# Kernel optimization log

Hardware: AMD Instinct MI355X
Metric: run time of the kernel (lower is better)

The kernel has to match this reference:

```python
import jax, jax.numpy as jnp
import numpy as np

Lx, Ly = 10, 10          # PEPS lattice (contract split at Lx//2 as in source)
PHYS, D, CHI = 2, 4, 4   # physical dim, bond dim, boundary max_bond (chi = D)


def setup_inputs() -> dict:
    key = jax.random.key(0)
    k1, k2 = jax.random.split(key)
    # scale so each site tensor has Frobenius norm ~1.5 (keeps the contraction
    # value inside float32 range; quimb handles this via equalize_norms=1.0)
    scale = 1.5 / np.sqrt(PHYS * D ** 4)
    peps = jax.random.normal(k1, (Lx, Ly, PHYS, D, D, D, D), dtype=jnp.float32) * scale
    x = jax.random.randint(k2, (Lx * Ly,), 0, PHYS, dtype=jnp.int32)
    return {"peps": peps, "x": x}


def _site(peps, x, i, j):
    # isel: select physical index; realize open boundary by slicing edge bonds to 1
    T = jnp.take(peps[i, j], x[i * Ly + j], axis=0)  # [Du, Dr, Dd, Dl]
    if i == Lx - 1:
        T = T[:1]
    if j == Ly - 1:
        T = T[:, :1]
    if i == 0:
        T = T[:, :, :1]
    if j == 0:
        T = T[:, :, :, :1]
    return T


def _compress(mps, chi):
    """Canonical MPS compression to bond dim chi (cutoff=0, canonize=True).
    Each tensor has legs (l, r, p) where p is the dangling (up/down) leg.
    Returns compressed MPS with tensor norms stripped into a log accumulator
    (equalize_norms=1.0 semantics; reabsorbed at the end)."""
    mps = list(mps)
    n = len(mps)
    # left-to-right QR canonization
    for j in range(n - 1):
        l, r, u = mps[j].shape
        M = mps[j].transpose(0, 2, 1).reshape(l * u, r)
        Q, R = jnp.linalg.qr(M)
        k = Q.shape[1]
        mps[j] = Q.reshape(l, u, k).transpose(0, 2, 1)
        mps[j + 1] = jnp.einsum('kr,rsu->ksu', R, mps[j + 1])
    # right-to-left truncating SVD sweep
    for j in range(n - 1, 0, -1):
        l, r, u = mps[j].shape
        M = mps[j].reshape(l, r * u)
        U, S, Vh = jnp.linalg.svd(M, full_matrices=False)
        k = min(chi, S.shape[0])
        mps[j] = Vh[:k].reshape(k, r, u)
        mps[j - 1] = jnp.einsum('lmu,mk->lku', mps[j - 1], U[:, :k] * S[:k])
    # equalize norms: strip per-tensor norms into an exponent
    logZ = jnp.zeros((), mps[0].dtype)
    for j in range(n):
        nrm = jnp.linalg.norm(mps[j])
        safe = jnp.where(nrm > 0, nrm, 1.0)
        mps[j] = mps[j] / safe
        logZ = logZ + jnp.log(safe)
    return mps, logZ


def _amp(peps, x):
    logZ = jnp.zeros((), peps.dtype)
    # bottom boundary MPS from row 0: site [U,R,d=1,L] -> (l, r, u)
    bot = [_site(peps, x, 0, j)[:, :, 0].transpose(2, 1, 0) for j in range(Ly)]
    for i in range(1, Lx // 2):  # contract_boundary_from_xmin_, xrange [0, Lx//2-1]
        row = []
        for j in range(Ly):
            T = _site(peps, x, i, j)      # [U, R, d, L]
            B = bot[j]                    # [l, r, u]
            C = jnp.einsum('lru,URuL->lLrRU', B, T)
            row.append(C.reshape(B.shape[0] * T.shape[3],
                                 B.shape[1] * T.shape[1], T.shape[0]))
        bot, lz = _compress(row, CHI)
        logZ = logZ + lz
    # top boundary MPS from row Lx-1: site [U=1,R,D,L] -> (l, r, d)
    top = [_site(peps, x, Lx - 1, j)[0].transpose(2, 0, 1) for j in range(Ly)]
    for i in range(Lx - 2, Lx // 2 - 1, -1):  # contract_boundary_from_xmax_
        row = []
        for j in range(Ly):
            T = _site(peps, x, i, j)      # [U, R, D, L]
            A = top[j]                    # [l, r, d]
            C = jnp.einsum('lrd,dRDL->lLrRD', A, T)
            row.append(C.reshape(A.shape[0] * T.shape[3],
                                 A.shape[1] * T.shape[1], T.shape[2]))
        top, lz = _compress(row, CHI)
        logZ = logZ + lz
    # zip the two boundary MPS across the central cut
    v = jnp.ones((1, 1), peps.dtype)
    for j in range(Ly):
        v = jnp.einsum('ab,apu,bqu->pq', v, bot[j], top[j])
    return v[0, 0] * jnp.exp(logZ)


def reference(peps, x):
    return _amp(peps, x)
```

## Files before the change

### kernel.cpp

```cpp
#include <hip/hip_runtime.h>
#include <math.h>


#define NS 10

__device__ __forceinline__ double shfl_d(double x, int src) {
  union { double d; int i[2]; } u;
  u.d = x;
  u.i[0] = __shfl(u.i[0], src, 64);
  u.i[1] = __shfl(u.i[1], src, 64);
  return u.d;
}
__device__ __forceinline__ double shflx_d(double x, int m) {
  union { double d; int i[2]; } u;
  u.d = x;
  u.i[0] = __shfl_xor(u.i[0], m, 64);
  u.i[1] = __shfl_xor(u.i[1], m, 64);
  return u.d;
}
__device__ __forceinline__ double wsum64(double x) {
#pragma unroll
  for (int o = 1; o < 64; o <<= 1) x += shflx_d(x, o);
  return x;
}
#define SEL4(a, k) ((k) == 1 ? (a)[1] : (k) == 2 ? (a)[2] : (k) == 3 ? (a)[3] : (a)[0])

template <int NDMAX>
__device__ void jacobi_sym_x(const double* gw, double* vtw, double* ev,
                             int lane, int maxsweep) {
  const int i = lane >> 2, j4 = lane & 3;
  double g[4], v[4];
#pragma unroll
  for (int cc = 0; cc < 4; ++cc) {
    g[cc] = gw[i * 16 + j4 * 4 + cc];
    v[cc] = (i == j4 * 4 + cc) ? 1.0 : 0.0;
  }
  for (int sw = 0; sw < maxsweep; ++sw) {
    double off = 0.0, dsq = 0.0;
#pragma unroll
    for (int cc = 0; cc < 4; ++cc) {
      double gv = g[cc];
      if (j4 * 4 + cc == i) dsq += gv * gv; else off += gv * gv;
    }
    off = wsum64(off); dsq = wsum64(dsq);
    if (off <= dsq * 1e-22) break;
#pragma unroll
    for (int d = 1; d <= NDMAX; ++d) {
      const int hb = d >= 8 ? 3 : d >= 4 ? 2 : d >= 2 ? 1 : 0;
      double dsel = SEL4(g, i & 3);
      double psel = SEL4(g, (i & 3) ^ (d & 3));
      double t1 = shfl_d(dsel, (i << 2) + (i >> 2));
      double t3 = shfl_d(psel, (i << 2) + ((i ^ d) >> 2));
      double t2 = shfl_d(dsel, ((i ^ d) << 2) + ((i ^ d) >> 2));
      bool iq = ((i >> hb) & 1) != 0;
      double th = iq ? (t1 - t2) : (t2 - t1);
      double ph = 2.0 * t3;
      double den = fabs(th) + sqrt(th * th + ph * ph);
      double t = (den > 0.0) ? copysign(1.0, th) * ph / den : 0.0;
      double cr = rsqrt(1.0 + t * t);
      double sr = t * cr;
      double oc[4], os[4], oth[4];
#pragma unroll
      for (int cc = 0; cc < 4; ++cc) {
        int col = (j4 << 2) + cc;
        int asrc = (col << 2) + (col >> 2);
        oc[cc] = shfl_d(cr, asrc);
        os[cc] = shfl_d(sr, asrc);
        oth[cc] = (d >> 2) ? shflx_d(g[cc ^ (d & 3)], d >> 2)
                           : g[cc ^ (d & 3)];
      }
#pragma unroll
      for (int cc = 0; cc < 4; ++cc) {
        int col = (j4 << 2) + cc;
        double sg = ((col >> hb) & 1) ? os[cc] : -os[cc];
        g[cc] = oc[cc] * g[cc] + sg * oth[cc];
      }
      double og[4], ov[4];
#pragma unroll
      for (int cc = 0; cc < 4; ++cc) og[cc] = shflx_d(g[cc], d << 2);
#pragma unroll
      for (int cc = 0; cc < 4; ++cc) ov[cc] = shflx_d(v[cc], d << 2);
      double sg2 = iq ? sr : -sr;
#pragma unroll
      for (int cc = 0; cc < 4; ++cc) {
        g[cc] = cr * g[cc] + sg2 * og[cc];
        v[cc] = cr * v[cc] + sg2 * ov[cc];
      }
    }
  }
#pragma unroll
  for (int cc = 0; cc < 4; ++cc) vtw[i * 16 + j4 * 4 + cc] = v[cc];
  if ((i >> 2) == j4) ev[i] = SEL4(g, i & 3);
}

__global__ __launch_bounds__(128, 1)
void amp_kernel(const float* __restrict__ peps, const int* __restrict__ xs,
                float* __restrict__ out) {
  const int tid = threadIdx.x;
  const int team = tid >> 6;
  const int lane = tid & 63;

  __shared__ __align__(16) float Ash[2][NS][1024];
  __shared__ __align__(16) float Tmp[2][1024];
  __shared__ __align__(16) float Tsh[2][256];
  __shared__ double Rw[2][256];
  __shared__ double Gw[2][256];
  __shared__ double Vt[2][256];
  __shared__ double USw[2][64];
  __shared__ double evals[2][16];
  __shared__ int dL[2][NS], dR[2][NS];
  __shared__ double lz[2];
  __shared__ double vbuf[2][16];

  float (*A)[1024] = Ash[team];
  float* tmp = Tmp[team];
  float* tsh = Tsh[team];
  double* rw = Rw[team];
  double* gw = Gw[team];
  double* vt = Vt[team];
  double* usw = USw[team];
  double* ev = evals[team];
  int* dl = dL[team];
  int* dr = dR[team];

  double logZ = 0.0;

  {
    int row0 = team ? 9 : 0;
    for (int j = 0; j < NS; ++j) {
      int p = xs[row0 * 10 + j];
      const float* tp = peps + ((size_t)(row0 * 10 + j) * 2 + p) * 256;
      ((float4*)tsh)[lane] = ((const float4*)tp)[lane];
      __syncthreads();
      int lgLt = (j == 0) ? 0 : 2, lgRt = (j == 9) ? 0 : 2;
      int Lt = 1 << lgLt, Rt = 1 << lgRt;
      int n = Lt * Rt * 4;
      if (lane < n) {
        int ui = lane & 3, h = lane >> 2;
        int ri = h & (Rt - 1), li = h >> lgRt;
        float val = team ? tsh[ri * 16 + ui * 4 + li]
                         : tsh[ui * 64 + ri * 16 + li];
        A[j][lane] = val;
      }
      if (lane == 0) { dl[j] = Lt; dr[j] = Rt; }
      __syncthreads();
    }
  }

  for (int it = 0; it < 4; ++it) {
    int row = team ? (8 - it) : (1 + it);

    for (int j = 0; j < NS; ++j) {
      int p = xs[row * 10 + j];
      const float* tp = peps + ((size_t)(row * 10 + j) * 2 + p) * 256;
      ((float4*)tsh)[lane] = ((const float4*)tp)[lane];
      int l = dl[j], r = dr[j];
      int nb = l * r * 4;
      for (int o = lane; o < nb; o += 64) tmp[o] = A[j][o];
      __syncthreads();
      int lgLt = (j == 0) ? 0 : 2, lgRt = (j == 9) ? 0 : 2;
      int lp = l << lgLt, rp = r << lgRt;
      int lgrp = 31 - __clz(rp);
      int n = lp * rp * 4;
      for (int o = lane; o < n; o += 64) {
        int U = o & 3;
        int h = o >> 2;
        int ro = h & (rp - 1), lo = h >> lgrp;
        int li = lo >> lgLt, Li = lo & ((1 << lgLt) - 1);
        int ri = ro >> lgRt, Ri = ro & ((1 << lgRt) - 1);
        double acc = 0.0;
#pragma unroll
        for (int w = 0; w < 4; ++w) {
          float b = tmp[(li * r + ri) * 4 + w];
          float t3 = team ? tsh[w * 64 + Ri * 16 + U * 4 + Li]
                          : tsh[U * 64 + Ri * 16 + w * 4 + Li];
          acc += (double)b * (double)t3;
        }
        A[j][o] = (float)acc;
      }
      if (lane == 0) { dl[j] = lp; dr[j] = rp; }
      __syncthreads();
    }

    for (int j = 0; j < NS - 1; ++j) {
      int l = dl[j], r = dr[j];
      int rows = l * 4, cols = r;
      int kq = rows < cols ? rows : cols;
      for (int o = lane; o < 256; o += 64) rw[o] = 0.0;
      double m[16];
      int li = lane >> 2, ui = lane & 3;
      bool act = lane < rows;
#pragma unroll
      for (int c = 0; c < 16; ++c)
        m[c] = (act && c < cols) ? (double)A[j][(li * r + c) * 4 + ui] : 0.0;
      __syncthreads();
#pragma unroll
      for (int c = 0; c < 16; ++c) {
        if (c < kq) {
          double rawd[16];
#pragma unroll
          for (int c2 = c; c2 < 16; ++c2)
            if (c2 < cols) rawd[c2] = wsum64(m[c] * m[c2]);
          double nrm = sqrt(rawd[c]);
          double inv = (nrm > 1e-150) ? 1.0 / nrm : 0.0;
          m[c] *= inv;
          if (lane == 0) rw[c * 16 + c] = nrm;
#pragma unroll
          for (int c2 = c + 1; c2 < 16; ++c2) {
            if (c2 < cols) {
              double dt = rawd[c2] * inv;
              m[c2] -= dt * m[c];
              if (lane == 0) rw[c * 16 + c2] = dt;
            }
          }
        }
      }
      if (act) {
#pragma unroll
        for (int c = 0; c < 16; ++c)
          if (c < kq) A[j][(li * kq + c) * 4 + ui] = (float)m[c];
      }
      if (lane == 0) dr[j] = kq;
      __syncthreads();
      int r2 = dr[j + 1];
      int ne = cols * r2 * 4;
      for (int o = lane; o < ne; o += 64) tmp[o] = A[j + 1][o];
      __syncthreads();
      int lgr2 = 31 - __clz(r2);
      int nout = kq * r2 * 4;
      for (int o = lane; o < nout; o += 64) {
        int u2 = o & 3;
        int h = o >> 2;
        int s = h & (r2 - 1), ki = h >> lgr2;
        double acc = 0.0;
        for (int c = ki; c < cols; ++c)
          acc += rw[ki * 16 + c] * (double)tmp[(c * r2 + s) * 4 + u2];
        A[j + 1][o] = (float)acc;
      }
      if (lane == 0) dl[j + 1] = kq;
      __syncthreads();
    }

    for (int j = NS - 1; j >= 1; --j) {
      int l = dl[j], r = dr[j], ru = r * 4;
      int mdim = l < ru ? l : ru;
      int k = mdim < 4 ? mdim : 4;
      bool caseA = (l <= ru);
      int d = caseA ? l : ru;
      for (int o = lane; o < 256; o += 64) gw[o] = 0.0;
      __syncthreads();
      if (caseA) {
        int lgl = 31 - __clz(l);
        for (int idx = lane; idx < l * l; idx += 64) {
          int a = idx >> lgl, b = idx & (l - 1);
          double acc = 0.0;
          for (int t2 = 0; t2 < ru; ++t2)
            acc += (double)A[j][a * ru + t2] * (double)A[j][b * ru + t2];
          gw[a * 16 + b] = acc;
        }
      } else {
        int lgru = 31 - __clz(ru);
        for (int idx = lane; idx < ru * ru; idx += 64) {
          int a = idx >> lgru, b = idx & (ru - 1);
          double acc = 0.0;
          for (int t2 = 0; t2 < l; ++t2)
            acc += (double)A[j][t2 * ru + a] * (double)A[j][t2 * ru + b];
          gw[a * 16 + b] = acc;
        }
      }
      __syncthreads();
      if (d > 4) jacobi_sym_x<15>(gw, vt, ev, lane, 10);
      else       jacobi_sym_x<3>(gw, vt, ev, lane, 6);
      __syncthreads();
      int idxs[4]; double sv[4];
      idxs[0] = idxs[1] = idxs[2] = idxs[3] = 0;
      sv[0] = sv[1] = sv[2] = sv[3] = 0.0;
      unsigned msk = 0;
#pragma unroll
      for (int t2 = 0; t2 < 4; ++t2) {
        if (t2 < k) {
          double best = -1.0; int bi = 0;
          for (int a = 0; a < 16; ++a) {
            double ea = ev[a];
            bool ok = !((msk >> a) & 1) && (ea > best);
            best = ok ? ea : best;
            bi = ok ? a : bi;
          }
          msk |= (1u << bi);
          idxs[t2] = bi;
          sv[t2] = sqrt(best > 0.0 ? best : 0.0);
        }
      }
      double vh[4] = {0.0, 0.0, 0.0, 0.0};
      if (caseA) {
        if (lane < ru) {
#pragma unroll
          for (int t2 = 0; t2 < 4; ++t2) if (t2 < k) {
            double acc = 0.0;
            for (int a = 0; a < l; ++a)
              acc += vt[idxs[t2] * 16 + a] * (double)A[j][a * ru + lane];
            double invs = sv[t2] > 1e-150 ? 1.0 / sv[t2] : 0.0;
            vh[t2] = acc * invs;
          }
        }
        if (lane < l) {
#pragma unroll
          for (int t2 = 0; t2 < 4; ++t2)
            usw[lane * 4 + t2] =
                (t2 < k) ? vt[idxs[t2] * 16 + lane] * sv[t2] : 0.0;
        }
      } else {
        if (lane < ru) {
#pragma unroll
          for (int t2 = 0; t2 < 4; ++t2)
            if (t2 < k) vh[t2] = vt[idxs[t2] * 16 + lane];
        }
        if (lane < l) {
#pragma unroll
          for (int t2 = 0; t2 < 4; ++t2) {
            double acc = 0.0;
            if (t2 < k)
              for (int q2 = 0; q2 < ru; ++q2)
                acc += (double)A[j][lane * ru + q2] * vt[idxs[t2] * 16 + q2];
            usw[lane * 4 + t2] = acc;
          }
        }
      }
      __syncthreads();
      if (lane < ru) {
#pragma unroll
        for (int t2 = 0; t2 < 4; ++t2)
          if (t2 < k) A[j][t2 * ru + lane] = (float)vh[t2];
      }
      if (lane == 0) dl[j] = k;
      __syncthreads();
      int l1 = dl[j - 1], r1 = dr[j - 1];
      int ne = l1 * r1 * 4;
      for (int o = lane; o < ne; o += 64) tmp[o] = A[j - 1][o];
      __syncthreads();
      int lgk = 31 - __clz(k);
      int nout = l1 * k * 4;
      for (int o = lane; o < nout; o += 64) {
        int u2 = o & 3;
        int h = o >> 2;
        int ki = h & (k - 1), li2 = h >> lgk;
        double acc = 0.0;
        for (int m2 = 0; m2 < l; ++m2)
          acc += (double)tmp[(li2 * l + m2) * 4 + u2] * usw[m2 * 4 + ki];
        A[j - 1][o] = (float)acc;
      }
      if (lane == 0) dr[j - 1] = k;
      __syncthreads();
    }

    for (int j = 0; j < NS; ++j) {
      int nels = dl[j] * dr[j] * 4;
      double part = 0.0;
      for (int o = lane; o < nels; o += 64) {
        double x = A[j][o];
        part += x * x;
      }
      double nrm = sqrt(wsum64(part));
      double safe = nrm > 0.0 ? nrm : 1.0;
      float invs = (float)(1.0 / safe);
      for (int o = lane; o < nels; o += 64) A[j][o] *= invs;
      logZ += log(safe);
      __syncthreads();
    }
  }

  if (lane == 0) lz[team] = logZ;
  if (tid < 16) vbuf[0][tid] = (tid == 0) ? 1.0 : 0.0;
  __syncthreads();
  int cur = 0;
  for (int j = 0; j < NS; ++j) {
    if (tid < 16) {
      int adim = dL[0][j], pdim = dR[0][j];
      int pp = tid >> 2, qq = tid & 3;
      double acc = 0.0;
      if (pp < pdim && qq < pdim) {
        for (int a = 0; a < adim; ++a)
          for (int b = 0; b < adim; ++b) {
            double vab = vbuf[cur][a * 4 + b];
            double s2 = 0.0;
#pragma unroll
            for (int u = 0; u < 4; ++u)
              s2 += (double)Ash[0][j][(a * pdim + pp) * 4 + u] *
                    (double)Ash[1][j][(b * pdim + qq) * 4 + u];
            acc += vab * s2;
          }
      }
      vbuf[cur ^ 1][tid] = acc;
    }
    __syncthreads();
    cur ^= 1;
  }
  if (tid == 0) out[0] = (float)(vbuf[cur][0] * exp(lz[0] + lz[1]));
}

extern "C" void kernel_launch(void* const* d_in, const int* in_sizes, int n_in,
                              void* d_out, int out_size, void* d_ws, size_t ws_size,
                              hipStream_t stream) {
  const float* peps = (const float*)d_in[0];
  const int* xs = (const int*)d_in[1];
  float* out = (float*)d_out;
  (void)in_sizes; (void)n_in; (void)out_size; (void)d_ws; (void)ws_size;
  amp_kernel<<<dim3(1), dim3(128), 0, stream>>>(peps, xs, out);
}
```

Baseline: 3.559 ms.

## Vectorize LDS accesses, split accumulators, cut Jacobi sweeps and convergence reductions

Several micro-optimizations go into the boundary-contraction kernel. Shared-memory copies and row contractions now use float4 loads, dot-product loops use four independent accumulators to shorten dependency chains, and the redundant zeroing of rw is dropped. The Jacobi eigen-solver computes its threshold once, needs only one wave reduction per sweep, and runs fewer maximum sweeps. Eigenvalues are cached in registers for top-k selection. Fewer sweeps and the looser convergence test may reduce accuracy of the truncated SVD.

```diff
diff --git a/kernel.cpp b/kernel.cpp
--- a/kernel.cpp
+++ b/kernel.cpp
@@ -35,6 +35,7 @@
     g[cc] = gw[i * 16 + j4 * 4 + cc];
     v[cc] = (i == j4 * 4 + cc) ? 1.0 : 0.0;
   }
+  double thr = 0.0;
   for (int sw = 0; sw < maxsweep; ++sw) {
     double off = 0.0, dsq = 0.0;
 #pragma unroll
@@ -42,8 +43,11 @@
       double gv = g[cc];
       if (j4 * 4 + cc == i) dsq += gv * gv; else off += gv * gv;
     }
-    off = wsum64(off); dsq = wsum64(dsq);
-    if (off <= dsq * 1e-22) break;
+    if (sw == 0) {
+      thr = wsum64(off + dsq) * 1e-16;
+    } else {
+      if (wsum64(off) <= thr) break;
+    }
 #pragma unroll
     for (int d = 1; d <= NDMAX; ++d) {
       const int hb = d >= 8 ? 3 : d >= 4 ? 2 : d >= 2 ? 1 : 0;
@@ -155,8 +159,9 @@
       const float* tp = peps + ((size_t)(row * 10 + j) * 2 + p) * 256;
       ((float4*)tsh)[lane] = ((const float4*)tp)[lane];
       int l = dl[j], r = dr[j];
-      int nb = l * r * 4;
-      for (int o = lane; o < nb; o += 64) tmp[o] = A[j][o];
+      int nb4 = (l * r * 4) >> 2;
+      for (int o = lane; o < nb4; o += 64)
+        ((float4*)tmp)[o] = ((const float4*)A[j])[o];
       __syncthreads();
       int lgLt = (j == 0) ? 0 : 2, lgRt = (j == 9) ? 0 : 2;
       int lp = l << lgLt, rp = r << lgRt;
@@ -168,13 +173,16 @@
         int ro = h & (rp - 1), lo = h >> lgrp;
         int li = lo >> lgLt, Li = lo & ((1 << lgLt) - 1);
         int ri = ro >> lgRt, Ri = ro & ((1 << lgRt) - 1);
-        double acc = 0.0;
-#pragma unroll
-        for (int w = 0; w < 4; ++w) {
-          float b = tmp[(li * r + ri) * 4 + w];
-          float t3 = team ? tsh[w * 64 + Ri * 16 + U * 4 + Li]
-                          : tsh[U * 64 + Ri * 16 + w * 4 + Li];
-          acc += (double)b * (double)t3;
+        const float4 bf = *(const float4*)&tmp[(li * r + ri) * 4];
+        double acc;
+        if (team) {
+          const float* tb = &tsh[Ri * 16 + U * 4 + Li];
+          acc = (double)bf.x * tb[0] + (double)bf.y * tb[64] +
+                (double)bf.z * tb[128] + (double)bf.w * tb[192];
+        } else {
+          const float* tb = &tsh[U * 64 + Ri * 16 + Li];
+          acc = (double)bf.x * tb[0] + (double)bf.y * tb[4] +
+                (double)bf.z * tb[8] + (double)bf.w * tb[12];
         }
         A[j][o] = (float)acc;
       }
@@ -186,7 +194,6 @@
       int l = dl[j], r = dr[j];
       int rows = l * 4, cols = r;
       int kq = rows < cols ? rows : cols;
-      for (int o = lane; o < 256; o += 64) rw[o] = 0.0;
       double m[16];
       int li = lane >> 2, ui = lane & 3;
       bool act = lane < rows;
@@ -223,19 +230,29 @@
       if (lane == 0) dr[j] = kq;
       __syncthreads();
       int r2 = dr[j + 1];
-      int ne = cols * r2 * 4;
-      for (int o = lane; o < ne; o += 64) tmp[o] = A[j + 1][o];
+      int ne4 = (cols * r2 * 4) >> 2;
+      for (int o = lane; o < ne4; o += 64)
+        ((float4*)tmp)[o] = ((const float4*)A[j + 1])[o];
       __syncthreads();
       int lgr2 = 31 - __clz(r2);
       int nout = kq * r2 * 4;
+      int stride = r2 * 4;
       for (int o = lane; o < nout; o += 64) {
         int u2 = o & 3;
         int h = o >> 2;
         int s = h & (r2 - 1), ki = h >> lgr2;
-        double acc = 0.0;
-        for (int c = ki; c < cols; ++c)
-          acc += rw[ki * 16 + c] * (double)tmp[(c * r2 + s) * 4 + u2];
-        A[j + 1][o] = (float)acc;
+        const double* rrow = &rw[ki * 16];
+        const float* tcol = &tmp[s * 4 + u2];
+        double s0 = 0.0, s1 = 0.0, s2 = 0.0, s3 = 0.0;
+        int c = ki;
+        for (; c + 4 <= cols; c += 4) {
+          s0 += rrow[c + 0] * (double)tcol[(c + 0) * stride];
+          s1 += rrow[c + 1] * (double)tcol[(c + 1) * stride];
+          s2 += rrow[c + 2] * (double)tcol[(c + 2) * stride];
+          s3 += rrow[c + 3] * (double)tcol[(c + 3) * stride];
+        }
+        for (; c < cols; ++c) s0 += rrow[c] * (double)tcol[c * stride];
+        A[j + 1][o] = (float)((s0 + s1) + (s2 + s3));
       }
       if (lane == 0) dl[j + 1] = kq;
       __syncthreads();
@@ -251,27 +268,45 @@
       __syncthreads();
       if (caseA) {
         int lgl = 31 - __clz(l);
+        int nq = ru >> 2;
         for (int idx = lane; idx < l * l; idx += 64) {
           int a = idx >> lgl, b = idx & (l - 1);
-          double acc = 0.0;
-          for (int t2 = 0; t2 < ru; ++t2)
-            acc += (double)A[j][a * ru + t2] * (double)A[j][b * ru + t2];
-          gw[a * 16 + b] = acc;
+          const float4* pa = (const float4*)&A[j][a * ru];
+          const float4* pb = (const float4*)&A[j][b * ru];
+          double s0 = 0.0, s1 = 0.0, s2 = 0.0, s3 = 0.0;
+          for (int q = 0; q < nq; ++q) {
+            float4 fa = pa[q], fb = pb[q];
+            s0 += (double)fa.x * fb.x;
+            s1 += (double)fa.y * fb.y;
+            s2 += (double)fa.z * fb.z;
+            s3 += (double)fa.w * fb.w;
+          }
+          gw[a * 16 + b] = (s0 + s1) + (s2 + s3);
         }
       } else {
         int lgru = 31 - __clz(ru);
         for (int idx = lane; idx < ru * ru; idx += 64) {
           int a = idx >> lgru, b = idx & (ru - 1);
-          double acc = 0.0;
-          for (int t2 = 0; t2 < l; ++t2)
-            acc += (double)A[j][t2 * ru + a] * (double)A[j][t2 * ru + b];
-          gw[a * 16 + b] = acc;
-        }
-      }
-      __syncthreads();
-      if (d > 4) jacobi_sym_x<15>(gw, vt, ev, lane, 10);
-      else       jacobi_sym_x<3>(gw, vt, ev, lane, 6);
-      __syncthreads();
+          double s0 = 0.0, s1 = 0.0, s2 = 0.0, s3 = 0.0;
+          int t2 = 0;
+          for (; t2 + 4 <= l; t2 += 4) {
+            s0 += (double)A[j][(t2 + 0) * ru + a] * A[j][(t2 + 0) * ru + b];
+            s1 += (double)A[j][(t2 + 1) * ru + a] * A[j][(t2 + 1) * ru + b];
+            s2 += (double)A[j][(t2 + 2) * ru + a] * A[j][(t2 + 2) * ru + b];
+            s3 += (double)A[j][(t2 + 3) * ru + a] * A[j][(t2 + 3) * ru + b];
+          }
+          for (; t2 < l; ++t2)
+            s0 += (double)A[j][t2 * ru + a] * A[j][t2 * ru + b];
+          gw[a * 16 + b] = (s0 + s1) + (s2 + s3);
+        }
+      }
+      __syncthreads();
+      if (d > 4) jacobi_sym_x<15>(gw, vt, ev, lane, 8);
+      else       jacobi_sym_x<3>(gw, vt, ev, lane, 5);
+      __syncthreads();
+      double evr[16];
+#pragma unroll
+      for (int a = 0; a < 16; ++a) evr[a] = ev[a];
       int idxs[4]; double sv[4];
       idxs[0] = idxs[1] = idxs[2] = idxs[3] = 0;
       sv[0] = sv[1] = sv[2] = sv[3] = 0.0;
@@ -280,8 +315,9 @@
       for (int t2 = 0; t2 < 4; ++t2) {
         if (t2 < k) {
           double best = -1.0; int bi = 0;
+#pragma unroll
           for (int a = 0; a < 16; ++a) {
-            double ea = ev[a];
+            double ea = evr[a];
             bool ok = !((msk >> a) & 1) && (ea > best);
             best = ok ? ea : best;
             bi = ok ? a : bi;
@@ -296,9 +332,17 @@
         if (lane < ru) {
 #pragma unroll
           for (int t2 = 0; t2 < 4; ++t2) if (t2 < k) {
-            double acc = 0.0;
-            for (int a = 0; a < l; ++a)
-              acc += vt[idxs[t2] * 16 + a] * (double)A[j][a * ru + lane];
+            const double* vrow = &vt[idxs[t2] * 16];
+            double s0 = 0.0, s1 = 0.0, s2 = 0.0, s3 = 0.0;
+            int a = 0;
+            for (; a + 4 <= l; a += 4) {
+              s0 += vrow[a + 0] * (double)A[j][(a + 0) * ru + lane];
+              s1 += vrow[a + 1] * (double)A[j][(a + 1) * ru + lane];
+              s2 += vrow[a + 2] * (double)A[j][(a + 2) * ru + lane];
+              s3 += vrow[a + 3] * (double)A[j][(a + 3) * ru + lane];
+            }
+            for (; a < l; ++a) s0 += vrow[a] * (double)A[j][a * ru + lane];
+            double acc = (s0 + s1) + (s2 + s3);
             double invs = sv[t2] > 1e-150 ? 1.0 / sv[t2] : 0.0;
             vh[t2] = acc * invs;
           }
@@ -319,9 +363,20 @@
 #pragma unroll
           for (int t2 = 0; t2 < 4; ++t2) {
             double acc = 0.0;
-            if (t2 < k)
-              for (int q2 = 0; q2 < ru; ++q2)
-                acc += (double)A[j][lane * ru + q2] * vt[idxs[t2] * 16 + q2];
+            if (t2 < k) {
+              const double* vrow = &vt[idxs[t2] * 16];
+              const float* arow = &A[j][lane * ru];
+              double s0 = 0.0, s1 = 0.0, s2 = 0.0, s3 = 0.0;
+              int q2 = 0;
+              for (; q2 + 4 <= ru; q2 += 4) {
+                s0 += (double)arow[q2 + 0] * vrow[q2 + 0];
+                s1 += (double)arow[q2 + 1] * vrow[q2 + 1];
+                s2 += (double)arow[q2 + 2] * vrow[q2 + 2];
+                s3 += (double)arow[q2 + 3] * vrow[q2 + 3];
+              }
+              for (; q2 < ru; ++q2) s0 += (double)arow[q2] * vrow[q2];
+              acc = (s0 + s1) + (s2 + s3);
+            }
             usw[lane * 4 + t2] = acc;
           }
         }
@@ -335,8 +390,9 @@
       if (lane == 0) dl[j] = k;
       __syncthreads();
       int l1 = dl[j - 1], r1 = dr[j - 1];
-      int ne = l1 * r1 * 4;
-      for (int o = lane; o < ne; o += 64) tmp[o] = A[j - 1][o];
+      int ne4 = (l1 * r1 * 4) >> 2;
+      for (int o = lane; o < ne4; o += 64)
+        ((float4*)tmp)[o] = ((const float4*)A[j - 1])[o];
       __syncthreads();
       int lgk = 31 - __clz(k);
       int nout = l1 * k * 4;
@@ -344,26 +400,39 @@
         int u2 = o & 3;
         int h = o >> 2;
         int ki = h & (k - 1), li2 = h >> lgk;
-        double acc = 0.0;
-        for (int m2 = 0; m2 < l; ++m2)
-          acc += (double)tmp[(li2 * l + m2) * 4 + u2] * usw[m2 * 4 + ki];
-        A[j - 1][o] = (float)acc;
+        const float* trow = &tmp[li2 * l * 4 + u2];
+        const double* ucol = &usw[ki];
+        double s0 = 0.0, s1 = 0.0, s2 = 0.0, s3 = 0.0;
+        int m2 = 0;
+        for (; m2 + 4 <= l; m2 += 4) {
+          s0 += (double)trow[(m2 + 0) * 4] * ucol[(m2 + 0) * 4];
+          s1 += (double)trow[(m2 + 1) * 4] * ucol[(m2 + 1) * 4];
+          s2 += (double)trow[(m2 + 2) * 4] * ucol[(m2 + 2) * 4];
+          s3 += (double)trow[(m2 + 3) * 4] * ucol[(m2 + 3) * 4];
+        }
+        for (; m2 < l; ++m2) s0 += (double)trow[m2 * 4] * ucol[m2 * 4];
+        A[j - 1][o] = (float)((s0 + s1) + (s2 + s3));
       }
       if (lane == 0) dr[j - 1] = k;
       __syncthreads();
     }
 
     for (int j = 0; j < NS; ++j) {
-      int nels = dl[j] * dr[j] * 4;
+      int n4 = (dl[j] * dr[j] * 4) >> 2;
       double part = 0.0;
-      for (int o = lane; o < nels; o += 64) {
-        double x = A[j][o];
-        part += x * x;
+      for (int o = lane; o < n4; o += 64) {
+        float4 v = ((const float4*)A[j])[o];
+        part += (double)v.x * v.x + (double)v.y * v.y +
+                (double)v.z * v.z + (double)v.w * v.w;
       }
       double nrm = sqrt(wsum64(part));
       double safe = nrm > 0.0 ? nrm : 1.0;
       float invs = (float)(1.0 / safe);
-      for (int o = lane; o < nels; o += 64) A[j][o] *= invs;
+      for (int o = lane; o < n4; o += 64) {
+        float4 v = ((float4*)A[j])[o];
+        v.x *= invs; v.y *= invs; v.z *= invs; v.w *= invs;
+        ((float4*)A[j])[o] = v;
+      }
       logZ += log(safe);
       __syncthreads();
     }
```

Result: faster. 3.437 ms (-3.4%).
